# Kernel tuning notes

Measured on AMD Instinct MI355X. Metric: run time of the kernel, lower is better.

Reference implementation:

```python
import jax, jax.numpy as jnp
import numpy as np

L = 2          # num_layers
D = 2048       # embed_dim
HQ = 16        # num_q_heads
HK = 4         # num_kv_heads
HD = D // HQ   # head_size = 128
G = HQ // HK   # q_to_kv_ratio = 4
P = 8192       # embed_dim_proj
V = 32000      # vocab_size
B = 1
S = 2048
EPS = 1e-5
THETA = 500000.0
NEG = -1e30


def setup_inputs() -> dict:
    key = jax.random.key(0)
    ks = jax.random.split(key, 8)
    s = 0.02
    return {
        "tokens": jax.random.randint(ks[0], (B, S), 0, V, dtype=jnp.int32),
        "embed": jax.random.normal(ks[1], (V, D), jnp.float32) * s,
        "attn_norm_w": jnp.ones((L, D), jnp.float32),
        "qkv_w": jax.random.normal(ks[2], (L, D, D + 2 * HK * HD), jnp.float32) * s,
        "attn_out_w": jax.random.normal(ks[3], (L, D, D), jnp.float32) * s,
        "mlp_norm_w": jnp.ones((L, D), jnp.float32),
        "mlp_in_w": jax.random.normal(ks[4], (L, D, 2 * P), jnp.float32) * s,
        "mlp_out_w": jax.random.normal(ks[5], (L, P, D), jnp.float32) * s,
        "final_norm_w": jnp.ones((D,), jnp.float32),
        "lm_head_w": jax.random.normal(ks[6], (D, V), jnp.float32) * s,
    }


def _rms(x, w):
    return w * (x * jax.lax.rsqrt(jnp.mean(x * x, axis=-1, keepdims=True) + EPS))


def _rope_cos_sin():
    inv = 1.0 / (THETA ** (jnp.arange(0, HD, 2, dtype=jnp.float32) / HD))  # [HD/2]
    ang = jnp.arange(S, dtype=jnp.float32)[:, None] * inv[None, :]         # [S, HD/2]
    return jnp.cos(ang), jnp.sin(ang)


def _rope(t, cos, sin):
    # t: [B,S,H,HD]; interleaved complex rotation on (even, odd) pairs
    x = t.reshape(t.shape[:-1] + (HD // 2, 2))
    x0, x1 = x[..., 0], x[..., 1]
    c = cos[None, :, None, :]
    sn = sin[None, :, None, :]
    out = jnp.stack([x0 * c - x1 * sn, x0 * sn + x1 * c], axis=-1)
    return out.reshape(t.shape)


def _layer(x, nw1, wqkv, wo, nw2, wi, wmo, cos, sin, mask):
    # attention block (pre-norm, residual)
    h = _rms(x, nw1)
    qkv = h @ wqkv
    q = qkv[..., :D].reshape(B, S, HQ, HD)
    k = qkv[..., D:D + HK * HD].reshape(B, S, HK, HD)
    v = qkv[..., D + HK * HD:].reshape(B, S, HK, HD)
    q = _rope(q, cos, sin)
    k = _rope(k, cos, sin)
    # GQA: repeat_interleave along head dim
    k = jnp.repeat(k, G, axis=2)
    v = jnp.repeat(v, G, axis=2)
    scores = jnp.einsum('bqhd,bkhd->bhqk', q, k) / np.float32(np.sqrt(HD))
    scores = jnp.where(mask, scores, NEG)
    attn = jax.nn.softmax(scores, axis=-1)
    o = jnp.einsum('bhqk,bkhd->bqhd', attn, v).reshape(B, S, D)
    x = x + o @ wo
    # SwiGLU block (pre-norm, residual)
    h = _rms(x, nw2)
    gu = h @ wi
    gate, up = gu[..., :P], gu[..., P:]
    x = x + (jax.nn.silu(gate) * up) @ wmo
    return x


def reference(tokens, embed, attn_norm_w, qkv_w, attn_out_w, mlp_norm_w,
              mlp_in_w, mlp_out_w, final_norm_w, lm_head_w):
    cos, sin = _rope_cos_sin()
    mask = jnp.tril(jnp.ones((S, S), dtype=bool))  # offset=0 prefill -> causal
    x = embed[tokens]  # [B,S,D]
    for i in range(L):
        x = _layer(x, attn_norm_w[i], qkv_w[i], attn_out_w[i],
                   mlp_norm_w[i], mlp_in_w[i], mlp_out_w[i], cos, sin, mask)
    return _rms(x, final_norm_w) @ lm_head_w  # [B,S,V]
```

## Files before the change

kernel.cpp:

```cpp
#include <hip/hip_runtime.h>
#include <math.h>

#define S_LEN 2048
#define DMODEL 2048
#define NHQ 16
#define NHK 4
#define HDIM 128
#define PDIM 8192
#define VOCAB 32000
#define NQKV 3072
#define EPSI 1e-5f

typedef unsigned short u16;
typedef unsigned int u32;
typedef __bf16 bf16x8 __attribute__((ext_vector_type(8)));
typedef float f32x4 __attribute__((ext_vector_type(4)));

__device__ __forceinline__ u16 f2bf(float f){
  u32 u = __builtin_bit_cast(u32, f);
  u += 0x7fffu + ((u >> 16) & 1u);
  return (u16)(u >> 16);
}
__device__ __forceinline__ float bf2f(u16 h){
  u32 u = ((u32)h) << 16;
  return __builtin_bit_cast(float, u);
}
__device__ __forceinline__ bf16x8 ld8(const u16* p){
  return __builtin_bit_cast(bf16x8, *(const uint4*)p);
}
__device__ __forceinline__ f32x4 mfma16(bf16x8 a, bf16x8 b, f32x4 c){
  return __builtin_amdgcn_mfma_f32_16x16x32_bf16(a, b, c, 0, 0, 0);
}

#define GLOAD_LDS16(gp, lp) __builtin_amdgcn_global_load_lds( \
    (__attribute__((address_space(1))) void*)(gp), \
    (__attribute__((address_space(3))) void*)(lp), 16, 0, 0)

__device__ __forceinline__ bf16x8 lds_frag(const u16* Lb, int R, int g){
  const int Rp = R >> 1;
  const int s8 = (((R & 1) << 2) | g) ^ (Rp & 7);
  return ld8(Lb + Rp * 64 + s8 * 8);
}
__device__ __forceinline__ void stage_sw(const u16* base, long row0, int K, int kt,
                                         int q, u16* Ldst_waveuniform){
  const int Rp = q >> 3;
  const int u = (q & 7) ^ (Rp & 7);
  const int R = (Rp << 1) | (u >> 2);
  const u16* gp = base + (row0 + R) * (long)K + kt + ((u & 3) << 3);
  GLOAD_LDS16(gp, Ldst_waveuniform);
}

__device__ __forceinline__ void map_bmn(int id0, int nwg, int nbn, int G,
                                        int& bm, int& bn){
  const int cpx = nwg >> 3;
  const int id = (id0 & 7) * cpx + (id0 >> 3);
  const int bmi = id % G;
  const int r2 = id / G;
  bn = r2 % nbn;
  bm = (r2 / nbn) * G + bmi;
}

__global__ void k_embed(const int* __restrict__ tok, const float* __restrict__ emb,
                        float* __restrict__ x){
  const int s = blockIdx.x, t = threadIdx.x;
  const long r = tok[s];
  const float4* src = (const float4*)(emb + r * DMODEL);
  float4* dst = (float4*)(x + (long)s * DMODEL);
  dst[t] = src[t];
  dst[t + 256] = src[t + 256];
}

__global__ void k_rmsnorm(const float* __restrict__ x, const float* __restrict__ w,
                          u16* __restrict__ out){
  const int s = blockIdx.x, t = threadIdx.x;
  const float4* xr = (const float4*)(x + (long)s * DMODEL);
  const float4 a = xr[t], b = xr[t + 256];
  float ss = a.x*a.x + a.y*a.y + a.z*a.z + a.w*a.w
           + b.x*b.x + b.y*b.y + b.z*b.z + b.w*b.w;
  #pragma unroll
  for (int off = 32; off > 0; off >>= 1) ss += __shfl_down(ss, off, 64);
  __shared__ float part[4];
  if ((t & 63) == 0) part[t >> 6] = ss;
  __syncthreads();
  const float r = rsqrtf((part[0] + part[1] + part[2] + part[3]) * (1.f / 2048.f) + EPSI);
  const float4* wr = (const float4*)w;
  const float4 wa = wr[t], wb = wr[t + 256];
  uint2 ua, ub;
  ua.x = (u32)f2bf(a.x*r*wa.x) | ((u32)f2bf(a.y*r*wa.y) << 16);
  ua.y = (u32)f2bf(a.z*r*wa.z) | ((u32)f2bf(a.w*r*wa.w) << 16);
  ub.x = (u32)f2bf(b.x*r*wb.x) | ((u32)f2bf(b.y*r*wb.y) << 16);
  ub.y = (u32)f2bf(b.z*r*wb.z) | ((u32)f2bf(b.w*r*wb.w) << 16);
  *(uint2*)(out + (long)s * DMODEL + 4 * t) = ua;
  *(uint2*)(out + (long)s * DMODEL + 1024 + 4 * t) = ub;
}

__global__ __launch_bounds__(256) void k_convT(const float* __restrict__ W,
                                               u16* __restrict__ Wt, int N, int K){
  const int n0 = blockIdx.x * 64, k0 = blockIdx.y * 64;
  const int t = threadIdx.x;
  __shared__ u16 T[64][72];
  const int r = t >> 4, c = (t & 15) << 2;
  #pragma unroll
  for (int p = 0; p < 4; ++p){
    const int k = p * 16 + r;
    const float4 v = *(const float4*)(W + (long)(k0 + k) * N + n0 + c);
    T[c + 0][k] = f2bf(v.x);
    T[c + 1][k] = f2bf(v.y);
    T[c + 2][k] = f2bf(v.z);
    T[c + 3][k] = f2bf(v.w);
  }
  __syncthreads();
  const int nr = t >> 3, kc = (t & 7) << 3;
  #pragma unroll
  for (int p = 0; p < 2; ++p){
    const int n = p * 32 + nr;
    *(uint4*)(Wt + (long)(n0 + n) * K + k0 + kc) = *(const uint4*)(&T[n][kc]);
  }
}

__global__ __launch_bounds__(256) void k_transV(const u16* __restrict__ qkv,
                                                u16* __restrict__ vT){
  const int s0 = blockIdx.x * 64, d0 = blockIdx.y * 64, kh = blockIdx.z;
  const int t = threadIdx.x;
  __shared__ u16 T[64][72];
  #pragma unroll
  for (int p = 0; p < 4; ++p){
    const int s = p * 16 + (t >> 4);
    const int c = (t & 15) * 4;
    const uint2 v = *(const uint2*)(qkv + (long)(s0 + s) * NQKV + DMODEL + 512 + kh * HDIM + d0 + c);
    T[c + 0][s] = (u16)(v.x);
    T[c + 1][s] = (u16)(v.x >> 16);
    T[c + 2][s] = (u16)(v.y);
    T[c + 3][s] = (u16)(v.y >> 16);
  }
  __syncthreads();
  #pragma unroll
  for (int p = 0; p < 2; ++p){
    const int d = p * 32 + (t >> 3);
    *(uint4*)(vT + ((long)kh * HDIM + d0 + d) * S_LEN + s0 + (t & 7) * 8) =
        *(const uint4*)(&T[d][(t & 7) * 8]);
  }
}

template<int OUT_BF16, int RES>
__global__ __launch_bounds__(256) void k_gemm(const u16* __restrict__ A, const u16* __restrict__ Bt,
                                              void* C, const float* Rs,
                                              int M, int N, int K, int nbn, int G){
  int bm, bn;
  map_bmn(blockIdx.x, gridDim.x, nbn, G, bm, bn);
  const int t = threadIdx.x;
  const int w = t >> 6, lane = t & 63, l15 = lane & 15, g = lane >> 4;
  const int wr = w >> 1, wc = w & 1;
  __shared__ u16 As[4096];
  __shared__ u16 Bs[4096];
  f32x4 acc[4][4] = {};
  const long arow = (long)bm * 128;
  const long brow = (long)bn * 128;
  for (int kt = 0; kt < K; kt += 32){
    __syncthreads();
    #pragma unroll
    for (int c = 0; c < 2; ++c){
      const int q0 = ((w << 1) | c) << 6;
      const int q  = q0 | lane;
      stage_sw(A,  arow, K, kt, q, As + q0 * 8);
      stage_sw(Bt, brow, K, kt, q, Bs + q0 * 8);
    }
    __syncthreads();
    bf16x8 af[4], bfr[4];
    #pragma unroll
    for (int i = 0; i < 4; ++i)
      af[i] = lds_frag(As, wr * 64 + i * 16 + l15, g);
    #pragma unroll
    for (int i = 0; i < 4; ++i)
      bfr[i] = lds_frag(Bs, wc * 64 + i * 16 + l15, g);
    #pragma unroll
    for (int mi = 0; mi < 4; ++mi)
      #pragma unroll
      for (int ni = 0; ni < 4; ++ni)
        acc[mi][ni] = mfma16(af[mi], bfr[ni], acc[mi][ni]);
  }
  const int row0 = bm * 128 + wr * 64, col0 = bn * 128 + wc * 64;
  #pragma unroll
  for (int mi = 0; mi < 4; ++mi){
    #pragma unroll
    for (int ni = 0; ni < 4; ++ni){
      #pragma unroll
      for (int r = 0; r < 4; ++r){
        const long ri = row0 + mi * 16 + g * 4 + r;
        const long ci = col0 + ni * 16 + l15;
        float v = acc[mi][ni][r];
        if (RES) v += Rs[ri * N + ci];
        if (OUT_BF16) ((u16*)C)[ri * N + ci] = f2bf(v);
        else          ((float*)C)[ri * N + ci] = v;
      }
    }
  }
}

template<int OUT_BF16>
__global__ __launch_bounds__(512, 2) void k_gemm256p(const u16* __restrict__ A,
                                                     const u16* __restrict__ Bt,
                                                     void* C, int M, int N, int K,
                                                     int nbn){
  __shared__ u16 L[65536];
  const int t = threadIdx.x;
  const int w = t >> 6, lane = t & 63, l15 = lane & 15, g = lane >> 4;
  const int wr = w >> 2, wc = w & 3;
  const int bm   = blockIdx.x & 7;
  const int slot = blockIdx.x >> 3;
  const int NT = K >> 5;

  const int Rp0 = t >> 3;
  const int u0  = (t & 7) ^ (Rp0 & 7);
  const int R0  = (Rp0 << 1) | (u0 >> 2);
  const int kcol0 = (u0 & 3) << 3;
  const u16* pA0base = A + ((long)bm * 256 + R0) * (long)K + kcol0;
  const u16* pA1base = pA0base + (long)128 * K;
  const int w0 = (t & ~63) * 8;

  for (int bn = slot; bn < nbn; bn += 32){
    const u16* pA0 = pA0base;
    const u16* pA1 = pA1base;
    const u16* pB0 = Bt + ((long)bn * 256 + R0) * (long)K + kcol0;
    const u16* pB1 = pB0 + (long)128 * K;

    auto stageA = [&](int s){
      u16* d = L + s * 8192;
      GLOAD_LDS16(pA0, d + w0); GLOAD_LDS16(pA1, d + 4096 + w0);
      pA0 += 32; pA1 += 32;
    };
    auto stageB = [&](int s){
      u16* d = L + 32768 + s * 8192;
      GLOAD_LDS16(pB0, d + w0); GLOAD_LDS16(pB1, d + 4096 + w0);
      pB0 += 32; pB1 += 32;
    };

    __builtin_amdgcn_s_barrier();
    stageA(0); stageB(0); stageA(1); stageB(1); stageA(2); stageB(2);
    asm volatile("s_waitcnt vmcnt(8)" ::: "memory");
    __builtin_amdgcn_s_barrier();

    f32x4 acc[8][4] = {};
    for (int tt = 0; tt < NT; ++tt){
      const u16* sA = L + (tt & 3) * 8192;
      const u16* sB = L + 32768 + (tt & 3) * 8192;
      bf16x8 af0[4], bfr[4];
      #pragma unroll
      for (int j = 0; j < 4; ++j)
        af0[j] = lds_frag(sA, wr * 128 + j * 16 + l15, g);
      #pragma unroll
      for (int n = 0; n < 4; ++n)
        bfr[n] = lds_frag(sB, wc * 64 + n * 16 + l15, g);
      if (tt + 3 < NT) stageA((tt + 3) & 3);
      asm volatile("s_waitcnt lgkmcnt(0)" ::: "memory");
      __builtin_amdgcn_s_barrier();
      __builtin_amdgcn_s_setprio(1);
      #pragma unroll
      for (int mi = 0; mi < 4; ++mi)
        #pragma unroll
        for (int ni = 0; ni < 4; ++ni)
          acc[mi][ni] = mfma16(af0[mi], bfr[ni], acc[mi][ni]);
      __builtin_amdgcn_s_setprio(0);
      bf16x8 af1[4];
      #pragma unroll
      for (int j = 0; j < 4; ++j)
        af1[j] = lds_frag(sA, wr * 128 + 64 + j * 16 + l15, g);
      if (tt + 3 < NT) stageB((tt + 3) & 3);
      asm volatile("s_waitcnt lgkmcnt(0)" ::: "memory");
      if (tt + 1 < NT){
        if (tt + 3 < NT)      asm volatile("s_waitcnt vmcnt(8)" ::: "memory");
        else if (tt + 2 < NT) asm volatile("s_waitcnt vmcnt(4)" ::: "memory");
        else                  asm volatile("s_waitcnt vmcnt(0)" ::: "memory");
      }
      __builtin_amdgcn_s_barrier();
      __builtin_amdgcn_s_setprio(1);
      #pragma unroll
      for (int mi = 0; mi < 4; ++mi)
        #pragma unroll
        for (int ni = 0; ni < 4; ++ni)
          acc[4 + mi][ni] = mfma16(af1[mi], bfr[ni], acc[4 + mi][ni]);
      __builtin_amdgcn_s_setprio(0);
    }
    const int row0 = bm * 256 + wr * 128, col0 = bn * 256 + wc * 64;
    #pragma unroll
    for (int mi = 0; mi < 8; ++mi){
      #pragma unroll
      for (int ni = 0; ni < 4; ++ni){
        #pragma unroll
        for (int r = 0; r < 4; ++r){
          const long ri = row0 + mi * 16 + g * 4 + r;
          const long ci = col0 + ni * 16 + l15;
          const float v = acc[mi][ni][r];
          if (OUT_BF16) ((u16*)C)[ri * N + ci] = f2bf(v);
          else          ((float*)C)[ri * N + ci] = v;
        }
      }
    }
  }
}

__global__ void k_rope(u16* __restrict__ qkv){
  const int idx = blockIdx.x * 256 + threadIdx.x;
  const int i = idx & 63;
  const int head = (idx >> 6) % 20;
  const int s = idx / (64 * 20);
  const long base = (long)s * NQKV + (head < NHQ ? head * HDIM : DMODEL + (head - NHQ) * HDIM);
  u32* p = (u32*)(qkv + base + 2 * i);
  const u32 v = *p;
  const float x0 = bf2f((u16)(v & 0xffffu)), x1 = bf2f((u16)(v >> 16));
  const float ang = (float)s * exp2f(-0.29580575889569023f * (float)i);
  float sn, cs;
  sincosf(ang, &sn, &cs);
  const float y0 = x0 * cs - x1 * sn;
  const float y1 = x0 * sn + x1 * cs;
  *p = (u32)f2bf(y0) | ((u32)f2bf(y1) << 16);
}

__global__ __launch_bounds__(256) void k_attn(const u16* __restrict__ qkv,
                                              const u16* __restrict__ vT,
                                              u16* __restrict__ o){
  const int id = blockIdx.x;
  const int xcd = id & 7, j = id >> 3;
  const int kh = xcd >> 1;
  const int h  = (kh << 2) + ((xcd & 1) << 1) + (j & 1);
  const int qb = 31 - (j >> 1);
  const int t = threadIdx.x, w = t >> 6, lane = t & 63, l15 = lane & 15, g = lane >> 4;
  __shared__ u16 Ks[2][8192];
  __shared__ u16 Vs[2][8192];
  __shared__ u16 Ps[4][16 * 72];
  const int q0 = qb * 64 + w * 16;
  bf16x8 aq[4];
  #pragma unroll
  for (int d0 = 0; d0 < 4; ++d0)
    aq[d0] = ld8(qkv + (long)(q0 + l15) * NQKV + h * HDIM + d0 * 32 + g * 8);
  f32x4 acc_o[8] = {};
  float mst[4], lst[4];
  #pragma unroll
  for (int r = 0; r < 4; ++r){ mst[r] = -1e30f; lst[r] = 0.f; }
  const float scale = 0.08838834764831843f;

  auto stageK = [&](int kt, int b){
    #pragma unroll
    for (int p = 0; p < 4; ++p){
      const int q = p * 256 + t;
      const int r = q >> 4, u = q & 15;
      const u16* gp = qkv + (long)(kt * 64 + r) * NQKV + DMODEL + kh * HDIM + ((u ^ (r & 15)) << 3);
      GLOAD_LDS16(gp, Ks[b] + (p * 256 + (t & ~63)) * 8);
    }
  };
  auto stageV = [&](int kt, int b){
    #pragma unroll
    for (int p = 0; p < 4; ++p){
      const int q = p * 256 + t;
      const int r = q >> 3, u = q & 7;
      const u16* gp = vT + ((long)kh * HDIM + r) * S_LEN + kt * 64 + ((u ^ (r & 7)) << 3);
      GLOAD_LDS16(gp, Vs[b] + (p * 256 + (t & ~63)) * 8);
    }
  };

  const int nkt = qb + 1;
  stageK(0, 0); stageV(0, 0);
  for (int kt = 0; kt < nkt; ++kt){
    const int kv0 = kt << 6;
    __builtin_amdgcn_s_barrier();
    if (kt + 1 < nkt){
      stageK(kt + 1, (kt + 1) & 1);
      stageV(kt + 1, (kt + 1) & 1);
      asm volatile("s_waitcnt vmcnt(8)" ::: "memory");
    } else {
      asm volatile("s_waitcnt vmcnt(0)" ::: "memory");
    }
    __builtin_amdgcn_s_barrier();
    const u16* K_ = Ks[kt & 1];
    const u16* V_ = Vs[kt & 1];
    f32x4 sacc[4] = {};
    #pragma unroll
    for (int d0 = 0; d0 < 4; ++d0){
      #pragma unroll
      for (int j2 = 0; j2 < 4; ++j2){
        const bf16x8 bk = ld8(K_ + (j2 * 16 + l15) * 128 + ((((d0 << 2) | g) ^ l15) << 3));
        sacc[j2] = mfma16(aq[d0], bk, sacc[j2]);
      }
    }
    float p[4][4], scl[4];
    #pragma unroll
    for (int r = 0; r < 4; ++r){
      const int qrow = q0 + g * 4 + r;
      float mx = -1e30f;
      #pragma unroll
      for (int j2 = 0; j2 < 4; ++j2){
        float sv = sacc[j2][r] * scale;
        sv = (kv0 + j2 * 16 + l15 <= qrow) ? sv : -1e30f;
        p[j2][r] = sv;
        mx = fmaxf(mx, sv);
      }
      #pragma unroll
      for (int off = 1; off < 16; off <<= 1) mx = fmaxf(mx, __shfl_xor(mx, off, 64));
      const float mnew = fmaxf(mst[r], mx);
      scl[r] = __expf(mst[r] - mnew);
      float rs = 0.f;
      #pragma unroll
      for (int j2 = 0; j2 < 4; ++j2){ p[j2][r] = __expf(p[j2][r] - mnew); rs += p[j2][r]; }
      #pragma unroll
      for (int off = 1; off < 16; off <<= 1) rs += __shfl_xor(rs, off, 64);
      lst[r] = lst[r] * scl[r] + rs;
      mst[r] = mnew;
    }
    #pragma unroll
    for (int n = 0; n < 8; ++n)
      #pragma unroll
      for (int r = 0; r < 4; ++r)
        acc_o[n][r] *= scl[r];
    #pragma unroll
    for (int j2 = 0; j2 < 4; ++j2)
      #pragma unroll
      for (int r = 0; r < 4; ++r)
        Ps[w][(g * 4 + r) * 72 + j2 * 16 + l15] = f2bf(p[j2][r]);
    #pragma unroll
    for (int kk = 0; kk < 2; ++kk){
      const bf16x8 pa = ld8(Ps[w] + l15 * 72 + kk * 32 + g * 8);
      #pragma unroll
      for (int n = 0; n < 8; ++n){
        const int row = n * 16 + l15;
        const bf16x8 bv = ld8(V_ + row * 64 + ((((kk << 2) | g) ^ (l15 & 7)) << 3));
        acc_o[n] = mfma16(pa, bv, acc_o[n]);
      }
    }
    asm volatile("s_waitcnt lgkmcnt(0)" ::: "memory");
  }
  #pragma unroll
  for (int n = 0; n < 8; ++n){
    #pragma unroll
    for (int r = 0; r < 4; ++r){
      const float ov = acc_o[n][r] / lst[r];
      o[(long)(q0 + g * 4 + r) * DMODEL + h * HDIM + n * 16 + l15] = f2bf(ov);
    }
  }
}

__global__ void k_swiglu(const u16* __restrict__ gu, u16* __restrict__ out){
  const long idx = ((long)blockIdx.x * 256 + threadIdx.x) * 8;
  const long s = idx >> 13;
  const int j = (int)(idx & 8191);
  const u16* gp = gu + s * 16384 + j;
  const uint4 gv = *(const uint4*)gp;
  const uint4 uv = *(const uint4*)(gp + PDIM);
  const u32 gw[4] = {gv.x, gv.y, gv.z, gv.w};
  const u32 uw[4] = {uv.x, uv.y, uv.z, uv.w};
  u32 ow[4];
  #pragma unroll
  for (int k = 0; k < 4; ++k){
    const float g0 = bf2f((u16)(gw[k] & 0xffffu)), g1 = bf2f((u16)(gw[k] >> 16));
    const float u0 = bf2f((u16)(uw[k] & 0xffffu)), u1 = bf2f((u16)(uw[k] >> 16));
    const float s0 = g0 / (1.f + __expf(-g0)) * u0;
    const float s1 = g1 / (1.f + __expf(-g1)) * u1;
    ow[k] = (u32)f2bf(s0) | ((u32)f2bf(s1) << 16);
  }
  uint4 ro; ro.x = ow[0]; ro.y = ow[1]; ro.z = ow[2]; ro.w = ow[3];
  *(uint4*)(out + idx) = ro;
}

extern "C" void kernel_launch(void* const* d_in, const int* in_sizes, int n_in,
                              void* d_out, int out_size, void* d_ws, size_t ws_size,
                              hipStream_t stream){
  const int*   tokens       = (const int*)d_in[0];
  const float* embed        = (const float*)d_in[1];
  const float* attn_norm_w  = (const float*)d_in[2];
  const float* qkv_w        = (const float*)d_in[3];
  const float* attn_out_w   = (const float*)d_in[4];
  const float* mlp_norm_w   = (const float*)d_in[5];
  const float* mlp_in_w     = (const float*)d_in[6];
  const float* mlp_out_w    = (const float*)d_in[7];
  const float* final_norm_w = (const float*)d_in[8];
  const float* lm_head_w    = (const float*)d_in[9];

  char* ws = (char*)d_ws;
  float* xf  = (float*)(ws);
  u16* hbf   = (u16*)(ws + 16777216);
  u16* qkvb  = (u16*)(ws + 25165824);
  u16* obf   = (u16*)(ws + 37748736);
  u16* gub   = (u16*)(ws + 46137344);
  u16* hb2   = (u16*)(ws + 113246208);
  u16* wbuf  = (u16*)(ws + 146800640);
  u16* vTb   = (u16*)(ws + 277872640);

  k_embed<<<S_LEN, 256, 0, stream>>>(tokens, embed, xf);
  for (int l = 0; l < 2; ++l){
    k_rmsnorm<<<S_LEN, 256, 0, stream>>>(xf, attn_norm_w + (long)l * DMODEL, hbf);
    k_convT<<<dim3(NQKV/64, DMODEL/64), 256, 0, stream>>>(
        qkv_w + (long)l * DMODEL * NQKV, wbuf, NQKV, DMODEL);
    k_gemm<1,0><<<(S_LEN/128) * (NQKV/128), 256, 0, stream>>>(
        hbf, wbuf, qkvb, nullptr, S_LEN, NQKV, DMODEL, NQKV/128, 4);
    k_rope<<<(S_LEN * 20 * 64) / 256, 256, 0, stream>>>(qkvb);
    k_transV<<<dim3(S_LEN/64, 2, 4), 256, 0, stream>>>(qkvb, vTb);
    k_attn<<<512, 256, 0, stream>>>(qkvb, vTb, obf);
    k_convT<<<dim3(DMODEL/64, DMODEL/64), 256, 0, stream>>>(
        attn_out_w + (long)l * DMODEL * DMODEL, wbuf, DMODEL, DMODEL);
    k_gemm<0,1><<<(S_LEN/128) * (DMODEL/128), 256, 0, stream>>>(
        obf, wbuf, xf, xf, S_LEN, DMODEL, DMODEL, DMODEL/128, 4);
    k_rmsnorm<<<S_LEN, 256, 0, stream>>>(xf, mlp_norm_w + (long)l * DMODEL, hbf);
    k_convT<<<dim3((2*PDIM)/64, DMODEL/64), 256, 0, stream>>>(
        mlp_in_w + (long)l * DMODEL * 2 * PDIM, wbuf, 2*PDIM, DMODEL);
    k_gemm256p<1><<<256, 512, 0, stream>>>(
        hbf, wbuf, gub, S_LEN, 2*PDIM, DMODEL, (2*PDIM)/256);
    k_swiglu<<<(S_LEN * PDIM / 8) / 256, 256, 0, stream>>>(gub, hb2);
    k_convT<<<dim3(DMODEL/64, PDIM/64), 256, 0, stream>>>(
        mlp_out_w + (long)l * PDIM * DMODEL, wbuf, DMODEL, PDIM);
    k_gemm<0,1><<<(S_LEN/128) * (DMODEL/128), 256, 0, stream>>>(
        hb2, wbuf, xf, xf, S_LEN, DMODEL, PDIM, DMODEL/128, 2);
  }
  k_rmsnorm<<<S_LEN, 256, 0, stream>>>(xf, final_norm_w, hbf);
  k_convT<<<dim3(VOCAB/64, DMODEL/64), 256, 0, stream>>>(lm_head_w, wbuf, VOCAB, DMODEL);
  k_gemm256p<0><<<256, 512, 0, stream>>>(
      hbf, wbuf, (float*)d_out, S_LEN, VOCAB, DMODEL, VOCAB/256);
}
```

Measured before the change: 1.575 ms.

## Replace persistent 256x256 GEMM with 256x128 tile kernel loading B into registers

Replaces the persistent 256x256-tile GEMM used for the MLP input projection and LM head with a non-persistent kernel using 256x128 tiles, one tile per block. Only A is staged through LDS in a 4-slot ring. Each wave loads its B fragments directly from global memory into double-buffered registers. This aims to cut LDS traffic and barriers and to raise block count, at the cost of less reuse of B per block and uncoalesced-looking direct global loads for B.

```diff
diff --git a/kernel.cpp b/kernel.cpp
--- a/kernel.cpp
+++ b/kernel.cpp
@@ -198,102 +198,83 @@
 }
 
 template<int OUT_BF16>
-__global__ __launch_bounds__(512, 2) void k_gemm256p(const u16* __restrict__ A,
-                                                     const u16* __restrict__ Bt,
-                                                     void* C, int M, int N, int K,
-                                                     int nbn){
-  __shared__ u16 L[65536];
+__global__ __launch_bounds__(512, 2) void k_gemmD(const u16* __restrict__ A,
+                                                  const u16* __restrict__ Bt,
+                                                  void* C, int M, int N){
+  const int KK = 2048;
+  __shared__ u16 As[4][8192];
   const int t = threadIdx.x;
   const int w = t >> 6, lane = t & 63, l15 = lane & 15, g = lane >> 4;
-  const int wr = w >> 2, wc = w & 3;
-  const int bm   = blockIdx.x & 7;
-  const int slot = blockIdx.x >> 3;
-  const int NT = K >> 5;
+  const int wr = w >> 1, wc = w & 1;
+  const int bm = blockIdx.x & 7;
+  const int bn = blockIdx.x >> 3;
+  const int NT = KK / 32;
 
   const int Rp0 = t >> 3;
   const int u0  = (t & 7) ^ (Rp0 & 7);
   const int R0  = (Rp0 << 1) | (u0 >> 2);
-  const int kcol0 = (u0 & 3) << 3;
-  const u16* pA0base = A + ((long)bm * 256 + R0) * (long)K + kcol0;
-  const u16* pA1base = pA0base + (long)128 * K;
+  const u16* pA0 = A + ((long)bm * 256 + R0) * KK + ((u0 & 3) << 3);
+  const u16* pA1 = pA0 + 128 * KK;
   const int w0 = (t & ~63) * 8;
 
-  for (int bn = slot; bn < nbn; bn += 32){
-    const u16* pA0 = pA0base;
-    const u16* pA1 = pA1base;
-    const u16* pB0 = Bt + ((long)bn * 256 + R0) * (long)K + kcol0;
-    const u16* pB1 = pB0 + (long)128 * K;
-
-    auto stageA = [&](int s){
-      u16* d = L + s * 8192;
-      GLOAD_LDS16(pA0, d + w0); GLOAD_LDS16(pA1, d + 4096 + w0);
-      pA0 += 32; pA1 += 32;
-    };
-    auto stageB = [&](int s){
-      u16* d = L + 32768 + s * 8192;
-      GLOAD_LDS16(pB0, d + w0); GLOAD_LDS16(pB1, d + 4096 + w0);
-      pB0 += 32; pB1 += 32;
-    };
-
-    __builtin_amdgcn_s_barrier();
-    stageA(0); stageB(0); stageA(1); stageB(1); stageA(2); stageB(2);
-    asm volatile("s_waitcnt vmcnt(8)" ::: "memory");
-    __builtin_amdgcn_s_barrier();
-
-    f32x4 acc[8][4] = {};
-    for (int tt = 0; tt < NT; ++tt){
-      const u16* sA = L + (tt & 3) * 8192;
-      const u16* sB = L + 32768 + (tt & 3) * 8192;
-      bf16x8 af0[4], bfr[4];
-      #pragma unroll
-      for (int j = 0; j < 4; ++j)
-        af0[j] = lds_frag(sA, wr * 128 + j * 16 + l15, g);
-      #pragma unroll
-      for (int n = 0; n < 4; ++n)
-        bfr[n] = lds_frag(sB, wc * 64 + n * 16 + l15, g);
-      if (tt + 3 < NT) stageA((tt + 3) & 3);
-      asm volatile("s_waitcnt lgkmcnt(0)" ::: "memory");
-      __builtin_amdgcn_s_barrier();
-      __builtin_amdgcn_s_setprio(1);
-      #pragma unroll
-      for (int mi = 0; mi < 4; ++mi)
-        #pragma unroll
-        for (int ni = 0; ni < 4; ++ni)
-          acc[mi][ni] = mfma16(af0[mi], bfr[ni], acc[mi][ni]);
-      __builtin_amdgcn_s_setprio(0);
-      bf16x8 af1[4];
-      #pragma unroll
-      for (int j = 0; j < 4; ++j)
-        af1[j] = lds_frag(sA, wr * 128 + 64 + j * 16 + l15, g);
-      if (tt + 3 < NT) stageB((tt + 3) & 3);
-      asm volatile("s_waitcnt lgkmcnt(0)" ::: "memory");
-      if (tt + 1 < NT){
-        if (tt + 3 < NT)      asm volatile("s_waitcnt vmcnt(8)" ::: "memory");
-        else if (tt + 2 < NT) asm volatile("s_waitcnt vmcnt(4)" ::: "memory");
-        else                  asm volatile("s_waitcnt vmcnt(0)" ::: "memory");
-      }
-      __builtin_amdgcn_s_barrier();
-      __builtin_amdgcn_s_setprio(1);
-      #pragma unroll
-      for (int mi = 0; mi < 4; ++mi)
-        #pragma unroll
-        for (int ni = 0; ni < 4; ++ni)
-          acc[4 + mi][ni] = mfma16(af1[mi], bfr[ni], acc[4 + mi][ni]);
-      __builtin_amdgcn_s_setprio(0);
-    }
-    const int row0 = bm * 256 + wr * 128, col0 = bn * 256 + wc * 64;
-    #pragma unroll
-    for (int mi = 0; mi < 8; ++mi){
-      #pragma unroll
-      for (int ni = 0; ni < 4; ++ni){
-        #pragma unroll
-        for (int r = 0; r < 4; ++r){
-          const long ri = row0 + mi * 16 + g * 4 + r;
-          const long ci = col0 + ni * 16 + l15;
-          const float v = acc[mi][ni][r];
-          if (OUT_BF16) ((u16*)C)[ri * N + ci] = f2bf(v);
-          else          ((float*)C)[ri * N + ci] = v;
-        }
+  const u16* pB = Bt + ((long)bn * 128 + wc * 64 + l15) * KK + g * 8;
+
+  auto stageA = [&](int slot){
+    GLOAD_LDS16(pA0, As[slot] + w0);
+    GLOAD_LDS16(pA1, As[slot] + 4096 + w0);
+    pA0 += 32; pA1 += 32;
+  };
+
+  stageA(0); stageA(1); stageA(2);
+  bf16x8 b0[4], b1[4];
+  #pragma unroll
+  for (int ni = 0; ni < 4; ++ni) b0[ni] = ld8(pB + ni * 16 * KK);
+  pB += 32;
+
+  f32x4 acc[4][4] = {};
+
+  #define TILE_STEP(tt, bc, bx)                                               \
+  {                                                                           \
+    if ((tt) + 1 < NT){                                                       \
+      _Pragma("unroll")                                                       \
+      for (int ni = 0; ni < 4; ++ni) bx[ni] = ld8(pB + ni * 16 * KK);         \
+      pB += 32;                                                               \
+    }                                                                         \
+    if ((tt) + 3 < NT) stageA(((tt) + 3) & 3);                                \
+    asm volatile("s_waitcnt vmcnt(8)" ::: "memory");                          \
+    __builtin_amdgcn_s_barrier();                                             \
+    bf16x8 af[4];                                                             \
+    _Pragma("unroll")                                                         \
+    for (int mi = 0; mi < 4; ++mi)                                            \
+      af[mi] = lds_frag(As[(tt) & 3], wr * 64 + mi * 16 + l15, g);            \
+    __builtin_amdgcn_s_setprio(1);                                            \
+    _Pragma("unroll")                                                         \
+    for (int mi = 0; mi < 4; ++mi)                                            \
+      _Pragma("unroll")                                                       \
+      for (int ni = 0; ni < 4; ++ni)                                          \
+        acc[mi][ni] = mfma16(af[mi], bc[ni], acc[mi][ni]);                    \
+    __builtin_amdgcn_s_setprio(0);                                            \
+    __builtin_amdgcn_s_barrier();                                             \
+  }
+
+  for (int tt = 0; tt < NT; tt += 2){
+    TILE_STEP(tt,     b0, b1);
+    TILE_STEP(tt + 1, b1, b0);
+  }
+  #undef TILE_STEP
+
+  const int row0 = bm * 256 + wr * 64, col0 = bn * 128 + wc * 64;
+  #pragma unroll
+  for (int mi = 0; mi < 4; ++mi){
+    #pragma unroll
+    for (int ni = 0; ni < 4; ++ni){
+      #pragma unroll
+      for (int r = 0; r < 4; ++r){
+        const long ri = row0 + mi * 16 + g * 4 + r;
+        const long ci = col0 + ni * 16 + l15;
+        const float v = acc[mi][ni][r];
+        if (OUT_BF16) ((u16*)C)[ri * N + ci] = f2bf(v);
+        else          ((float*)C)[ri * N + ci] = v;
       }
     }
   }
@@ -501,8 +482,8 @@
     k_rmsnorm<<<S_LEN, 256, 0, stream>>>(xf, mlp_norm_w + (long)l * DMODEL, hbf);
     k_convT<<<dim3((2*PDIM)/64, DMODEL/64), 256, 0, stream>>>(
         mlp_in_w + (long)l * DMODEL * 2 * PDIM, wbuf, 2*PDIM, DMODEL);
-    k_gemm256p<1><<<256, 512, 0, stream>>>(
-        hbf, wbuf, gub, S_LEN, 2*PDIM, DMODEL, (2*PDIM)/256);
+    k_gemmD<1><<<8 * ((2*PDIM)/128), 512, 0, stream>>>(
+        hbf, wbuf, gub, S_LEN, 2*PDIM);
     k_swiglu<<<(S_LEN * PDIM / 8) / 256, 256, 0, stream>>>(gub, hb2);
     k_convT<<<dim3(DMODEL/64, PDIM/64), 256, 0, stream>>>(
         mlp_out_w + (long)l * PDIM * DMODEL, wbuf, DMODEL, PDIM);
@@ -511,6 +492,6 @@
   }
   k_rmsnorm<<<S_LEN, 256, 0, stream>>>(xf, final_norm_w, hbf);
   k_convT<<<dim3(VOCAB/64, DMODEL/64), 256, 0, stream>>>(lm_head_w, wbuf, VOCAB, DMODEL);
-  k_gemm256p<0><<<256, 512, 0, stream>>>(
-      hbf, wbuf, (float*)d_out, S_LEN, VOCAB, DMODEL, VOCAB/256);
-}
+  k_gemmD<0><<<8 * (VOCAB/128), 512, 0, stream>>>(
+      hbf, wbuf, (float*)d_out, S_LEN, VOCAB);
+}
```

New measurement: 2.347 ms. 49.0% more time.

## Split-K the MLP down-projection and launch non-persistent 256-tile GEMMs

Applied to the files above, without the earlier changes.

The MLP output GEMM (K=8192) is split into two K halves by a new simple kernel that writes fp32 partials into the gate/up buffer. A separate kernel then adds both partials into the residual. This doubles the number of workgroups and aims to fill more CUs. The 256x256 GEMM changes from a persistent loop over column tiles to one tile per block with an XCD-aware tile remap, and the attention launch drops its XCD-aware, heavy-first head and query-block order for a plain 2D grid. The costs are extra fp32 partial traffic and an extra launch, a split-K kernel with no multi-stage pipelining, and lost scheduling locality in attention.

```diff
diff --git a/kernel.cpp b/kernel.cpp
--- a/kernel.cpp
+++ b/kernel.cpp
@@ -41,12 +41,12 @@
   const int s8 = (((R & 1) << 2) | g) ^ (Rp & 7);
   return ld8(Lb + Rp * 64 + s8 * 8);
 }
-__device__ __forceinline__ void stage_sw(const u16* base, long row0, int K, int kt,
+__device__ __forceinline__ void stage_sw(const u16* base, long row0, int kstride, int kt,
                                          int q, u16* Ldst_waveuniform){
   const int Rp = q >> 3;
   const int u = (q & 7) ^ (Rp & 7);
   const int R = (Rp << 1) | (u >> 2);
-  const u16* gp = base + (row0 + R) * (long)K + kt + ((u & 3) << 3);
+  const u16* gp = base + (row0 + R) * (long)kstride + kt + ((u & 3) << 3);
   GLOAD_LDS16(gp, Ldst_waveuniform);
 }
 
@@ -197,103 +197,167 @@
   }
 }
 
+__global__ __launch_bounds__(256) void k_gemmsk(const u16* __restrict__ A,
+                                                const u16* __restrict__ Bt,
+                                                float* __restrict__ P,
+                                                int M, int N, int K, int nbn, int G){
+  const int ks = blockIdx.y;
+  const int KH = K >> 1;
+  A  += (long)ks * KH;
+  Bt += (long)ks * KH;
+  P  += (long)ks * M * N;
+  int bm, bn;
+  map_bmn(blockIdx.x, gridDim.x, nbn, G, bm, bn);
+  const int t = threadIdx.x;
+  const int w = t >> 6, lane = t & 63, l15 = lane & 15, g = lane >> 4;
+  const int wr = w >> 1, wc = w & 1;
+  __shared__ u16 As[4096];
+  __shared__ u16 Bs[4096];
+  f32x4 acc[4][4] = {};
+  const long arow = (long)bm * 128;
+  const long brow = (long)bn * 128;
+  for (int kt = 0; kt < KH; kt += 32){
+    __syncthreads();
+    #pragma unroll
+    for (int c = 0; c < 2; ++c){
+      const int q0 = ((w << 1) | c) << 6;
+      const int q  = q0 | lane;
+      stage_sw(A,  arow, K, kt, q, As + q0 * 8);
+      stage_sw(Bt, brow, K, kt, q, Bs + q0 * 8);
+    }
+    __syncthreads();
+    bf16x8 af[4], bfr[4];
+    #pragma unroll
+    for (int i = 0; i < 4; ++i)
+      af[i] = lds_frag(As, wr * 64 + i * 16 + l15, g);
+    #pragma unroll
+    for (int i = 0; i < 4; ++i)
+      bfr[i] = lds_frag(Bs, wc * 64 + i * 16 + l15, g);
+    #pragma unroll
+    for (int mi = 0; mi < 4; ++mi)
+      #pragma unroll
+      for (int ni = 0; ni < 4; ++ni)
+        acc[mi][ni] = mfma16(af[mi], bfr[ni], acc[mi][ni]);
+  }
+  const int row0 = bm * 128 + wr * 64, col0 = bn * 128 + wc * 64;
+  #pragma unroll
+  for (int mi = 0; mi < 4; ++mi){
+    #pragma unroll
+    for (int ni = 0; ni < 4; ++ni){
+      #pragma unroll
+      for (int r = 0; r < 4; ++r){
+        const long ri = row0 + mi * 16 + g * 4 + r;
+        const long ci = col0 + ni * 16 + l15;
+        P[ri * N + ci] = acc[mi][ni][r];
+      }
+    }
+  }
+}
+
+__global__ void k_red2(float* __restrict__ x, const float* __restrict__ p0,
+                       const float* __restrict__ p1){
+  const long i = ((long)blockIdx.x * 256 + threadIdx.x) * 4;
+  const float4 a = *(const float4*)(p0 + i);
+  const float4 b = *(const float4*)(p1 + i);
+  float4 c = *(const float4*)(x + i);
+  c.x += a.x + b.x; c.y += a.y + b.y; c.z += a.z + b.z; c.w += a.w + b.w;
+  *(float4*)(x + i) = c;
+}
+
 template<int OUT_BF16>
-__global__ __launch_bounds__(512, 2) void k_gemm256p(const u16* __restrict__ A,
-                                                     const u16* __restrict__ Bt,
-                                                     void* C, int M, int N, int K,
-                                                     int nbn){
+__global__ __launch_bounds__(512, 2) void k_gemm256(const u16* __restrict__ A,
+                                                    const u16* __restrict__ Bt,
+                                                    void* C, int M, int N, int K){
   __shared__ u16 L[65536];
   const int t = threadIdx.x;
   const int w = t >> 6, lane = t & 63, l15 = lane & 15, g = lane >> 4;
   const int wr = w >> 2, wc = w & 3;
-  const int bm   = blockIdx.x & 7;
-  const int slot = blockIdx.x >> 3;
+  const int nbm = M >> 8;
+  int id = blockIdx.x;
+  {
+    const int cpx = gridDim.x >> 3;
+    id = (id & 7) * cpx + (id >> 3);
+  }
+  const int bm = id % nbm, bn = id / nbm;
   const int NT = K >> 5;
 
   const int Rp0 = t >> 3;
   const int u0  = (t & 7) ^ (Rp0 & 7);
   const int R0  = (Rp0 << 1) | (u0 >> 2);
-  const int kcol0 = (u0 & 3) << 3;
-  const u16* pA0base = A + ((long)bm * 256 + R0) * (long)K + kcol0;
-  const u16* pA1base = pA0base + (long)128 * K;
+  const u16* pA0 = A  + ((long)bm * 256 + R0) * (long)K + ((u0 & 3) << 3);
+  const u16* pB0 = Bt + ((long)bn * 256 + R0) * (long)K + ((u0 & 3) << 3);
+  const u16* pA1 = pA0 + (long)128 * K;
+  const u16* pB1 = pB0 + (long)128 * K;
   const int w0 = (t & ~63) * 8;
 
-  for (int bn = slot; bn < nbn; bn += 32){
-    const u16* pA0 = pA0base;
-    const u16* pA1 = pA1base;
-    const u16* pB0 = Bt + ((long)bn * 256 + R0) * (long)K + kcol0;
-    const u16* pB1 = pB0 + (long)128 * K;
-
-    auto stageA = [&](int s){
-      u16* d = L + s * 8192;
-      GLOAD_LDS16(pA0, d + w0); GLOAD_LDS16(pA1, d + 4096 + w0);
-      pA0 += 32; pA1 += 32;
-    };
-    auto stageB = [&](int s){
-      u16* d = L + 32768 + s * 8192;
-      GLOAD_LDS16(pB0, d + w0); GLOAD_LDS16(pB1, d + 4096 + w0);
-      pB0 += 32; pB1 += 32;
-    };
-
+  auto stageA = [&](int s){
+    u16* d = L + s * 8192;
+    GLOAD_LDS16(pA0, d + w0); GLOAD_LDS16(pA1, d + 4096 + w0);
+    pA0 += 32; pA1 += 32;
+  };
+  auto stageB = [&](int s){
+    u16* d = L + 32768 + s * 8192;
+    GLOAD_LDS16(pB0, d + w0); GLOAD_LDS16(pB1, d + 4096 + w0);
+    pB0 += 32; pB1 += 32;
+  };
+
+  stageA(0); stageB(0); stageA(1); stageB(1); stageA(2); stageB(2);
+  asm volatile("s_waitcnt vmcnt(8)" ::: "memory");
+  __builtin_amdgcn_s_barrier();
+
+  f32x4 acc[8][4] = {};
+  for (int tt = 0; tt < NT; ++tt){
+    const u16* sA = L + (tt & 3) * 8192;
+    const u16* sB = L + 32768 + (tt & 3) * 8192;
+    bf16x8 af0[4], bfr[4];
+    #pragma unroll
+    for (int j = 0; j < 4; ++j)
+      af0[j] = lds_frag(sA, wr * 128 + j * 16 + l15, g);
+    #pragma unroll
+    for (int n = 0; n < 4; ++n)
+      bfr[n] = lds_frag(sB, wc * 64 + n * 16 + l15, g);
+    if (tt + 3 < NT) stageA((tt + 3) & 3);
+    asm volatile("s_waitcnt lgkmcnt(0)" ::: "memory");
     __builtin_amdgcn_s_barrier();
-    stageA(0); stageB(0); stageA(1); stageB(1); stageA(2); stageB(2);
-    asm volatile("s_waitcnt vmcnt(8)" ::: "memory");
+    __builtin_amdgcn_s_setprio(1);
+    #pragma unroll
+    for (int mi = 0; mi < 4; ++mi)
+      #pragma unroll
+      for (int ni = 0; ni < 4; ++ni)
+        acc[mi][ni] = mfma16(af0[mi], bfr[ni], acc[mi][ni]);
+    __builtin_amdgcn_s_setprio(0);
+    bf16x8 af1[4];
+    #pragma unroll
+    for (int j = 0; j < 4; ++j)
+      af1[j] = lds_frag(sA, wr * 128 + 64 + j * 16 + l15, g);
+    if (tt + 3 < NT) stageB((tt + 3) & 3);
+    asm volatile("s_waitcnt lgkmcnt(0)" ::: "memory");
+    if (tt + 1 < NT){
+      if (tt + 3 < NT)      asm volatile("s_waitcnt vmcnt(8)" ::: "memory");
+      else if (tt + 2 < NT) asm volatile("s_waitcnt vmcnt(4)" ::: "memory");
+      else                  asm volatile("s_waitcnt vmcnt(0)" ::: "memory");
+    }
     __builtin_amdgcn_s_barrier();
-
-    f32x4 acc[8][4] = {};
-    for (int tt = 0; tt < NT; ++tt){
-      const u16* sA = L + (tt & 3) * 8192;
-      const u16* sB = L + 32768 + (tt & 3) * 8192;
-      bf16x8 af0[4], bfr[4];
-      #pragma unroll
-      for (int j = 0; j < 4; ++j)
-        af0[j] = lds_frag(sA, wr * 128 + j * 16 + l15, g);
-      #pragma unroll
-      for (int n = 0; n < 4; ++n)
-        bfr[n] = lds_frag(sB, wc * 64 + n * 16 + l15, g);
-      if (tt + 3 < NT) stageA((tt + 3) & 3);
-      asm volatile("s_waitcnt lgkmcnt(0)" ::: "memory");
-      __builtin_amdgcn_s_barrier();
-      __builtin_amdgcn_s_setprio(1);
-      #pragma unroll
-      for (int mi = 0; mi < 4; ++mi)
-        #pragma unroll
-        for (int ni = 0; ni < 4; ++ni)
-          acc[mi][ni] = mfma16(af0[mi], bfr[ni], acc[mi][ni]);
-      __builtin_amdgcn_s_setprio(0);
-      bf16x8 af1[4];
-      #pragma unroll
-      for (int j = 0; j < 4; ++j)
-        af1[j] = lds_frag(sA, wr * 128 + 64 + j * 16 + l15, g);
-      if (tt + 3 < NT) stageB((tt + 3) & 3);
-      asm volatile("s_waitcnt lgkmcnt(0)" ::: "memory");
-      if (tt + 1 < NT){
-        if (tt + 3 < NT)      asm volatile("s_waitcnt vmcnt(8)" ::: "memory");
-        else if (tt + 2 < NT) asm volatile("s_waitcnt vmcnt(4)" ::: "memory");
-        else                  asm volatile("s_waitcnt vmcnt(0)" ::: "memory");
-      }
-      __builtin_amdgcn_s_barrier();
-      __builtin_amdgcn_s_setprio(1);
-      #pragma unroll
-      for (int mi = 0; mi < 4; ++mi)
-        #pragma unroll
-        for (int ni = 0; ni < 4; ++ni)
-          acc[4 + mi][ni] = mfma16(af1[mi], bfr[ni], acc[4 + mi][ni]);
-      __builtin_amdgcn_s_setprio(0);
-    }
-    const int row0 = bm * 256 + wr * 128, col0 = bn * 256 + wc * 64;
-    #pragma unroll
-    for (int mi = 0; mi < 8; ++mi){
-      #pragma unroll
-      for (int ni = 0; ni < 4; ++ni){
-        #pragma unroll
-        for (int r = 0; r < 4; ++r){
-          const long ri = row0 + mi * 16 + g * 4 + r;
-          const long ci = col0 + ni * 16 + l15;
-          const float v = acc[mi][ni][r];
-          if (OUT_BF16) ((u16*)C)[ri * N + ci] = f2bf(v);
-          else          ((float*)C)[ri * N + ci] = v;
-        }
+    __builtin_amdgcn_s_setprio(1);
+    #pragma unroll
+    for (int mi = 0; mi < 4; ++mi)
+      #pragma unroll
+      for (int ni = 0; ni < 4; ++ni)
+        acc[4 + mi][ni] = mfma16(af1[mi], bfr[ni], acc[4 + mi][ni]);
+    __builtin_amdgcn_s_setprio(0);
+  }
+  const int row0 = bm * 256 + wr * 128, col0 = bn * 256 + wc * 64;
+  #pragma unroll
+  for (int mi = 0; mi < 8; ++mi){
+    #pragma unroll
+    for (int ni = 0; ni < 4; ++ni){
+      #pragma unroll
+      for (int r = 0; r < 4; ++r){
+        const long ri = row0 + mi * 16 + g * 4 + r;
+        const long ci = col0 + ni * 16 + l15;
+        const float v = acc[mi][ni][r];
+        if (OUT_BF16) ((u16*)C)[ri * N + ci] = f2bf(v);
+        else          ((float*)C)[ri * N + ci] = v;
       }
     }
   }
@@ -319,11 +383,8 @@
 __global__ __launch_bounds__(256) void k_attn(const u16* __restrict__ qkv,
                                               const u16* __restrict__ vT,
                                               u16* __restrict__ o){
-  const int id = blockIdx.x;
-  const int xcd = id & 7, j = id >> 3;
-  const int kh = xcd >> 1;
-  const int h  = (kh << 2) + ((xcd & 1) << 1) + (j & 1);
-  const int qb = 31 - (j >> 1);
+  const int qb = blockIdx.x, h = blockIdx.y;
+  const int kh = h >> 2;
   const int t = threadIdx.x, w = t >> 6, lane = t & 63, l15 = lane & 15, g = lane >> 4;
   __shared__ u16 Ks[2][8192];
   __shared__ u16 Vs[2][8192];
@@ -483,6 +544,7 @@
   u16* hb2   = (u16*)(ws + 113246208);
   u16* wbuf  = (u16*)(ws + 146800640);
   u16* vTb   = (u16*)(ws + 277872640);
+  float* pp  = (float*)gub;
 
   k_embed<<<S_LEN, 256, 0, stream>>>(tokens, embed, xf);
   for (int l = 0; l < 2; ++l){
@@ -493,7 +555,7 @@
         hbf, wbuf, qkvb, nullptr, S_LEN, NQKV, DMODEL, NQKV/128, 4);
     k_rope<<<(S_LEN * 20 * 64) / 256, 256, 0, stream>>>(qkvb);
     k_transV<<<dim3(S_LEN/64, 2, 4), 256, 0, stream>>>(qkvb, vTb);
-    k_attn<<<512, 256, 0, stream>>>(qkvb, vTb, obf);
+    k_attn<<<dim3(S_LEN/64, NHQ), 256, 0, stream>>>(qkvb, vTb, obf);
     k_convT<<<dim3(DMODEL/64, DMODEL/64), 256, 0, stream>>>(
         attn_out_w + (long)l * DMODEL * DMODEL, wbuf, DMODEL, DMODEL);
     k_gemm<0,1><<<(S_LEN/128) * (DMODEL/128), 256, 0, stream>>>(
@@ -501,16 +563,18 @@
     k_rmsnorm<<<S_LEN, 256, 0, stream>>>(xf, mlp_norm_w + (long)l * DMODEL, hbf);
     k_convT<<<dim3((2*PDIM)/64, DMODEL/64), 256, 0, stream>>>(
         mlp_in_w + (long)l * DMODEL * 2 * PDIM, wbuf, 2*PDIM, DMODEL);
-    k_gemm256p<1><<<256, 512, 0, stream>>>(
-        hbf, wbuf, gub, S_LEN, 2*PDIM, DMODEL, (2*PDIM)/256);
+    k_gemm256<1><<<(S_LEN/256) * ((2*PDIM)/256), 512, 0, stream>>>(
+        hbf, wbuf, gub, S_LEN, 2*PDIM, DMODEL);
     k_swiglu<<<(S_LEN * PDIM / 8) / 256, 256, 0, stream>>>(gub, hb2);
     k_convT<<<dim3(DMODEL/64, PDIM/64), 256, 0, stream>>>(
         mlp_out_w + (long)l * PDIM * DMODEL, wbuf, DMODEL, PDIM);
-    k_gemm<0,1><<<(S_LEN/128) * (DMODEL/128), 256, 0, stream>>>(
-        hb2, wbuf, xf, xf, S_LEN, DMODEL, PDIM, DMODEL/128, 2);
+    k_gemmsk<<<dim3((S_LEN/128) * (DMODEL/128), 2), 256, 0, stream>>>(
+        hb2, wbuf, pp, S_LEN, DMODEL, PDIM, DMODEL/128, 2);
+    k_red2<<<(S_LEN * DMODEL) / 1024, 256, 0, stream>>>(
+        xf, pp, pp + (long)S_LEN * DMODEL);
   }
   k_rmsnorm<<<S_LEN, 256, 0, stream>>>(xf, final_norm_w, hbf);
   k_convT<<<dim3(VOCAB/64, DMODEL/64), 256, 0, stream>>>(lm_head_w, wbuf, VOCAB, DMODEL);
-  k_gemm256p<0><<<256, 512, 0, stream>>>(
-      hbf, wbuf, (float*)d_out, S_LEN, VOCAB, DMODEL, VOCAB/256);
-}
+  k_gemm256<0><<<(S_LEN/256) * (VOCAB/256), 512, 0, stream>>>(
+      hbf, wbuf, (float*)d_out, S_LEN, VOCAB, DMODEL);
+}
```

Result: faster. 1.416 ms (-10.1%).
